# Performance work log

Measured on AMD Instinct MI355X. Metric: run time of the kernel, lower is better.

Reference implementation:

```python
import jax, jax.numpy as jnp
import numpy as np


def setup_inputs() -> dict:
    key = jax.random.key(0)
    ks = jax.random.split(key, 6)
    B, S, D_IN, D_OUT = 4, 2048, 1024, 1024
    return {
        "inputs_for_keys": jax.random.normal(ks[0], (B, S, D_IN), dtype=jnp.float32),
        "inputs_for_values": jax.random.normal(ks[1], (B, S, D_IN), dtype=jnp.float32),
        "inputs_for_queries": jax.random.normal(ks[2], (B, S, D_IN), dtype=jnp.float32),
        "K_weight": jax.random.normal(ks[3], (D_IN, D_OUT), dtype=jnp.float32) * 0.1,
        "V_weight": jax.random.normal(ks[4], (D_IN, D_OUT), dtype=jnp.float32) * 0.1,
        "Q_weight": jax.random.normal(ks[5], (D_IN, D_OUT), dtype=jnp.float32) * 0.1,
    }


def reference(inputs_for_keys, inputs_for_values, inputs_for_queries,
              K_weight, V_weight, Q_weight):
    # QKV projections: [B,S,D_in] @ [D_in,D_out] -> [B,S,D_out]
    K = jnp.einsum("bsi,io->bso", inputs_for_keys, K_weight)
    V = jnp.einsum("bsi,io->bso", inputs_for_values, V_weight)
    Q = jnp.einsum("bsi,io->bso", inputs_for_queries, Q_weight)

    Sq, Sk, d = Q.shape[1], K.shape[1], K.shape[2]
    scale = 1.0 / jnp.sqrt(jnp.asarray(d, dtype=Q.dtype))
    # scaled dot-product scores: [B, Sq, Sk]
    scores = jnp.einsum("bqd,bkd->bqk", Q, K) * scale
    # causal mask: -inf strictly above the diagonal (key index > query index)
    causal = jnp.where(jnp.arange(Sk)[None, :] > jnp.arange(Sq)[:, None],
                       jnp.float32(-jnp.inf), jnp.float32(0.0))
    scores = scores + causal[None, :, :]
    probs = jax.nn.softmax(scores, axis=-1)
    return jnp.einsum("bqk,bkd->bqd", probs, V)
```

## Files before the change

kernel.cpp:

```cpp
#include <hip/hip_runtime.h>
#include <math.h>

using f32x4  = __attribute__((ext_vector_type(4))) float;
using bf16x8 = __attribute__((ext_vector_type(8))) short;
using f16x8  = __attribute__((ext_vector_type(8))) _Float16;
using u16x8  = __attribute__((ext_vector_type(8))) unsigned short;
using u16x4  = __attribute__((ext_vector_type(4))) unsigned short;

static __device__ __forceinline__ unsigned short f2bf(float f) {
  unsigned int u = __builtin_bit_cast(unsigned int, f);
  u += 0x7FFFu + ((u >> 16) & 1u);
  return (unsigned short)(u >> 16);
}
static __device__ __forceinline__ float bf2f(unsigned short h) {
  unsigned int u = ((unsigned int)h) << 16;
  return __builtin_bit_cast(float, u);
}
static __device__ __forceinline__ unsigned short f2h(float f) {
  _Float16 h = (_Float16)f;
  return __builtin_bit_cast(unsigned short, h);
}

template <bool F16>
static __device__ __forceinline__ f32x4 mfma16(bf16x8 a, bf16x8 b, f32x4 c) {
  if constexpr (F16)
    return __builtin_amdgcn_mfma_f32_16x16x32_f16(
        __builtin_bit_cast(f16x8, a), __builtin_bit_cast(f16x8, b), c, 0, 0, 0);
  else
    return __builtin_amdgcn_mfma_f32_16x16x32_bf16(a, b, c, 0, 0, 0);
}
template <bool F16>
static __device__ __forceinline__ unsigned short cvt16(float v) {
  if constexpr (F16) return f2h(v);
  else return f2bf(v);
}

static __device__ __forceinline__ void gll16(const void* g, void* l) {
  using GPtr = const unsigned int __attribute__((address_space(1)))*;
  using LPtr = unsigned int __attribute__((address_space(3)))*;
  __builtin_amdgcn_global_load_lds((GPtr)(unsigned long long)g,
                                   (LPtr)(unsigned)(unsigned long long)l,
                                   16, 0, 0);
}

template <int BK>
static __device__ __forceinline__ void stageT(unsigned short* sdst,
                                              const unsigned short* g,
                                              size_t ld, int k0, int wave,
                                              int lane) {
  if constexpr (BK == 64) {
    const int r = lane >> 3, c8 = lane & 7;
    const int scol = (c8 ^ r) << 3;
#pragma unroll
    for (int i = 0; i < 4; ++i)
      gll16(g + (size_t)(wave * 32 + i * 8 + r) * ld + (k0 + scol),
            sdst + wave * 2048 + i * 512);
  } else {
    const int p = lane & 7;
    const int ll = lane >> 3;
#pragma unroll
    for (int i = 0; i < 2; ++i) {
      const int line = wave * 16 + i * 8 + ll;
      const int q = p ^ (line & 7);
      const int srow = 2 * line + (q >> 2);
      const int scol = (q & 3) << 3;
      gll16(g + (size_t)srow * ld + (k0 + scol), sdst + wave * 1024 + i * 512);
    }
  }
}

template <int BK>
static __device__ __forceinline__ bf16x8 fragT(const unsigned short* s,
                                               int row, int kko) {
  if constexpr (BK == 64) {
    return *(const bf16x8*)&s[row * 64 + (kko ^ ((row & 7) << 3))];
  } else {
    const int line = row >> 1;
    const int q = ((row & 1) << 2) | (kko >> 3);
    const int p = q ^ (line & 7);
    return *(const bf16x8*)&s[line * 64 + p * 8];
  }
}

__global__ __launch_bounds__(256) void convert_wkq_kernel(
    const float* __restrict__ Wk, const float* __restrict__ Wq,
    unsigned short* __restrict__ Wkh, unsigned short* __restrict__ Wqh) {
  const int z = blockIdx.z;
  const float* W = z ? Wq : Wk;
  unsigned short* H = z ? Wqh : Wkh;
  const size_t base = (size_t)blockIdx.x * 4096 + threadIdx.x * 4;
#pragma unroll
  for (int k = 0; k < 4; ++k) {
    f32x4 v = *(const f32x4*)&W[base + k * 1024];
    u16x4 h;
#pragma unroll
    for (int e = 0; e < 4; ++e) h[e] = f2h(v[e]);
    *(u16x4*)&H[base + k * 1024] = h;
  }
}

__global__ __launch_bounds__(256) void convert_wv_kernel(
    const float* __restrict__ Wv, unsigned short* __restrict__ WvT) {
  __shared__ float sW[64][65];
  const int ti = blockIdx.x * 64;
  const int tj = blockIdx.y * 64;
  const int tid = threadIdx.x;
#pragma unroll
  for (int it = 0; it < 4; ++it) {
    int idx = tid + it * 256;
    int r = idx >> 4, c = (idx & 15) << 2;
    f32x4 v = *(const f32x4*)&Wv[(size_t)(ti + r) * 1024 + tj + c];
    sW[r][c] = v[0]; sW[r][c + 1] = v[1]; sW[r][c + 2] = v[2]; sW[r][c + 3] = v[3];
  }
  __syncthreads();
#pragma unroll
  for (int it = 0; it < 4; ++it) {
    int idx = tid + it * 256;
    int ro = idx >> 4, ci = (idx & 15) << 2;
    u16x4 h;
#pragma unroll
    for (int e = 0; e < 4; ++e) h[e] = f2h(sW[ci + e][ro]);
    *(u16x4*)&WvT[(size_t)(tj + ro) * 1024 + ti + ci] = h;
  }
}

__global__ __launch_bounds__(256) void convert_x_kernel(
    const float* __restrict__ Xk, const float* __restrict__ Xq,
    const float* __restrict__ Xv, unsigned short* __restrict__ Xkh,
    unsigned short* __restrict__ Xqh, unsigned short* __restrict__ Xvh) {
  const int z = blockIdx.z;
  const float* X = (z == 0) ? Xk : (z == 1) ? Xq : Xv;
  unsigned short* H = (z == 0) ? Xkh : (z == 1) ? Xqh : Xvh;
  const size_t base = (size_t)blockIdx.x * 4096 + threadIdx.x * 4;
#pragma unroll
  for (int k = 0; k < 4; ++k) {
    f32x4 v = *(const f32x4*)&X[base + k * 1024];
    u16x4 h;
#pragma unroll
    for (int e = 0; e < 4; ++e) h[e] = f2h(v[e]);
    *(u16x4*)&H[base + k * 1024] = h;
  }
}

template <int NTERMS, int EPI, bool PACKED, bool PVK, bool F16>
__global__ __launch_bounds__(256, 2) void gemm_db_kernel(
    const unsigned short* __restrict__ Ah, const unsigned short* __restrict__ Al,
    const unsigned short* __restrict__ Bh, const unsigned short* __restrict__ Bl,
    size_t lda, size_t ldb, int K,
    float* __restrict__ Cf, unsigned short* __restrict__ Ch,
    unsigned short* __restrict__ Cl, size_t ldc,
    size_t abatch, size_t bbatch, size_t cbatch) {
  constexpr int BK = (NTERMS >= 2) ? 32 : 64;
  constexpr int NTILES = (NTERMS == 3) ? 4 : (NTERMS == 2) ? 3 : 2;
  constexpr int TILE = 128 * BK;
  __shared__ unsigned short smem[2][NTILES * TILE];

  int lid = blockIdx.x + gridDim.x * (blockIdx.y + gridDim.y * blockIdx.z);
  {
    const int n = gridDim.x * gridDim.y * gridDim.z;
    const int q = n >> 3, r = n & 7, x = lid & 7, k = lid >> 3;
    lid = (x < r ? x * (q + 1) : r * (q + 1) + (x - r) * q) + k;
  }
  int bm, bn, b;
  if constexpr (PACKED) {
    const int t = lid % gridDim.x;
    b = lid / gridDim.x;
    bm = (int)((sqrtf(8.f * (float)t + 1.f) - 1.f) * 0.5f);
    while ((bm + 1) * (bm + 2) / 2 <= t) ++bm;
    while (bm * (bm + 1) / 2 > t) --bm;
    bn = t - bm * (bm + 1) / 2;
  } else {
    bn = lid % gridDim.x;
    const int tmp = lid / gridDim.x;
    bm = tmp % gridDim.y;
    b = tmp / gridDim.y;
    if constexpr (PVK) bm = (int)gridDim.y - 1 - bm;
  }
  const int tid = threadIdx.x, lane = tid & 63, wave = tid >> 6;
  const unsigned short* gA = Ah + abatch * b + (size_t)(bm * 128) * lda;
  const unsigned short* gB = Bh + bbatch * b + (size_t)(bn * 128) * ldb;
  const unsigned short* gAl2 =
      (NTERMS == 3) ? Al + abatch * b + (size_t)(bm * 128) * lda : nullptr;
  const unsigned short* gBl2 =
      (NTERMS >= 2) ? Bl + bbatch * b + (size_t)(bn * 128) * ldb : nullptr;
  const int kend = PVK ? (bm + 1) * 128 : K;
  const int nsteps = kend / BK;
  f32x4 acc[4][4] = {};
  const int wr = (wave >> 1) << 6, wc = (wave & 1) << 6;
  const int frow = lane & 15, koff = (lane >> 4) << 3;

  auto stage_all = [&](unsigned short* buf, int k0) {
    stageT<BK>(buf, gA, lda, k0, wave, lane);
    stageT<BK>(buf + TILE, gB, ldb, k0, wave, lane);
    if constexpr (NTERMS >= 2) stageT<BK>(buf + 2 * TILE, gBl2, ldb, k0, wave, lane);
    if constexpr (NTERMS == 3) stageT<BK>(buf + 3 * TILE, gAl2, lda, k0, wave, lane);
  };

  stage_all(smem[0], 0);
  if (nsteps > 1) stage_all(smem[1], BK);
  int cur = 0;
  for (int st = 0; st < nsteps; ++st) {
    if (st + 1 < nsteps) {
      if constexpr (NTERMS == 2)
        asm volatile("s_waitcnt vmcnt(6)" ::: "memory");
      else
        asm volatile("s_waitcnt vmcnt(8)" ::: "memory");
    } else {
      asm volatile("s_waitcnt vmcnt(0)" ::: "memory");
    }
    __builtin_amdgcn_sched_barrier(0);
    __builtin_amdgcn_s_barrier();
    __builtin_amdgcn_sched_barrier(0);
    const unsigned short* sA = smem[cur];
    const unsigned short* sB = smem[cur] + TILE;
    if constexpr (NTERMS >= 2) {
      const unsigned short* sBl = smem[cur] + 2 * TILE;
      const unsigned short* sAl = smem[cur] + 3 * TILE;
      bf16x8 fBh[4], fBl[4];
#pragma unroll
      for (int j = 0; j < 4; ++j) {
        fBh[j] = fragT<BK>(sB, wc + j * 16 + frow, koff);
        fBl[j] = fragT<BK>(sBl, wc + j * 16 + frow, koff);
      }
#pragma unroll
      for (int i = 0; i < 4; ++i) {
        const bf16x8 ah = fragT<BK>(sA, wr + i * 16 + frow, koff);
        bf16x8 al = {};
        if constexpr (NTERMS == 3) al = fragT<BK>(sAl, wr + i * 16 + frow, koff);
#pragma unroll
        for (int j = 0; j < 4; ++j) {
          acc[i][j] = mfma16<F16>(ah, fBh[j], acc[i][j]);
          acc[i][j] = mfma16<F16>(ah, fBl[j], acc[i][j]);
          if constexpr (NTERMS == 3)
            acc[i][j] = mfma16<F16>(al, fBh[j], acc[i][j]);
        }
      }
    } else {
#pragma unroll
      for (int kk = 0; kk < 64; kk += 32) {
        const int kko = kk + koff;
        bf16x8 fBh[4];
#pragma unroll
        for (int j = 0; j < 4; ++j) fBh[j] = fragT<BK>(sB, wc + j * 16 + frow, kko);
#pragma unroll
        for (int i = 0; i < 4; ++i) {
          const bf16x8 ah = fragT<BK>(sA, wr + i * 16 + frow, kko);
#pragma unroll
          for (int j = 0; j < 4; ++j)
            acc[i][j] = mfma16<F16>(ah, fBh[j], acc[i][j]);
        }
      }
    }
    asm volatile("s_waitcnt lgkmcnt(0)" ::: "memory");
    __builtin_amdgcn_sched_barrier(0);
    __builtin_amdgcn_s_barrier();
    __builtin_amdgcn_sched_barrier(0);
    if (st + 2 < nsteps) stage_all(smem[cur], (st + 2) * BK);
    cur ^= 1;
  }

  const int erow = bm * 128 + wr + ((lane >> 4) << 2);
  const int ecol = bn * 128 + wc + frow;
  if constexpr (EPI == 0) {
    float* C = Cf + cbatch * b;
#pragma unroll
    for (int i = 0; i < 4; ++i)
#pragma unroll
      for (int j = 0; j < 4; ++j)
#pragma unroll
        for (int e = 0; e < 4; ++e)
          C[(size_t)(erow + i * 16 + e) * ldc + (ecol + j * 16)] = acc[i][j][e];
  } else if constexpr (EPI == 3) {
#pragma unroll
    for (int i = 0; i < 4; ++i)
#pragma unroll
      for (int j = 0; j < 4; ++j) {
        const int s = erow + i * 16;
        const int o = ecol + j * 16;
        u16x4 v;
#pragma unroll
        for (int e = 0; e < 4; ++e) v[e] = cvt16<F16>(acc[i][j][e]);
        *(u16x4*)&Ch[((size_t)(s >> 11) * 1024 + o) * 2048 + (s & 2047)] = v;
      }
  } else {
    unsigned short* Cho = Ch + cbatch * b;
    unsigned short* Clo = (EPI == 1) ? Cl + cbatch * b : nullptr;
#pragma unroll
    for (int i = 0; i < 4; ++i)
#pragma unroll
      for (int j = 0; j < 4; ++j)
#pragma unroll
        for (int e = 0; e < 4; ++e) {
          size_t off = (size_t)(erow + i * 16 + e) * ldc + (ecol + j * 16);
          float v = acc[i][j][e];
          unsigned short hh = cvt16<F16>(v);
          Cho[off] = hh;
          if constexpr (EPI == 1) Clo[off] = f2bf(v - bf2f(hh));
        }
  }
}

__global__ __launch_bounds__(256) void reduce_mt_kernel(
    const float* __restrict__ P, unsigned short* __restrict__ H) {
  const size_t base = ((size_t)blockIdx.x * 256 + threadIdx.x) * 4;
  f32x4 s = *(const f32x4*)&P[base];
#pragma unroll
  for (int z = 1; z < 4; ++z) {
    f32x4 v = *(const f32x4*)&P[(size_t)z * 1048576 + base];
    s[0] += v[0]; s[1] += v[1]; s[2] += v[2]; s[3] += v[3];
  }
  u16x4 h;
#pragma unroll
  for (int e = 0; e < 4; ++e) h[e] = f2h(s[e]);
  *(u16x4*)&H[base] = h;
}

__global__ __launch_bounds__(256) void softmax_kernel(float* __restrict__ Sc) {
  const int row = blockIdx.x;
  const int q = row & 2047;
  const int tid = threadIdx.x, lane = tid & 63, wave = tid >> 6;
  float* srow = Sc + (size_t)row * 2048;
  unsigned short* prow = (unsigned short*)srow;
  const int k0 = tid * 4, k1 = 1024 + tid * 4;
  f32x4 v0 = {}, v1 = {};
  if (k0 <= q) v0 = *(const f32x4*)(srow + k0);
  if (k1 <= q) v1 = *(const f32x4*)(srow + k1);
  float m = -3.0e38f;
#pragma unroll
  for (int e = 0; e < 4; ++e) {
    if (k0 + e <= q) m = fmaxf(m, v0[e]);
    if (k1 + e <= q) m = fmaxf(m, v1[e]);
  }
#pragma unroll
  for (int o = 32; o; o >>= 1) m = fmaxf(m, __shfl_xor(m, o));
  __shared__ float redm[4], reds[4];
  if (lane == 0) redm[wave] = m;
  __syncthreads();
  m = fmaxf(fmaxf(redm[0], redm[1]), fmaxf(redm[2], redm[3]));
  const float scale = 0.03125f;
  float p[8];
  float s = 0.f;
#pragma unroll
  for (int e = 0; e < 4; ++e) {
    p[e] = (k0 + e <= q) ? __expf((v0[e] - m) * scale) : 0.f;
    p[4 + e] = (k1 + e <= q) ? __expf((v1[e] - m) * scale) : 0.f;
    s += p[e] + p[4 + e];
  }
#pragma unroll
  for (int o = 32; o; o >>= 1) s += __shfl_xor(s, o);
  if (lane == 0) reds[wave] = s;
  __syncthreads();
  s = reds[0] + reds[1] + reds[2] + reds[3];
  const float inv = 1.0f / s;
  u16x4 o0, o1;
#pragma unroll
  for (int e = 0; e < 4; ++e) {
    o0[e] = f2h(p[e] * inv);
    o1[e] = f2h(p[4 + e] * inv);
  }
  *(u16x4*)&prow[k0] = o0;
  *(u16x4*)&prow[k1] = o1;
}

extern "C" void kernel_launch(void* const* d_in, const int* in_sizes, int n_in,
                              void* d_out, int out_size, void* d_ws, size_t ws_size,
                              hipStream_t stream) {
  const float* Xk = (const float*)d_in[0];
  const float* Xv = (const float*)d_in[1];
  const float* Xq = (const float*)d_in[2];
  const float* Wk = (const float*)d_in[3];
  const float* Wv = (const float*)d_in[4];
  const float* Wq = (const float*)d_in[5];
  float* out = (float*)d_out;

  char* ws = (char*)d_ws;
  const size_t MB = 1024ull * 1024;
  unsigned short* Xqh   = (unsigned short*)(ws + 0);
  unsigned short* Xvh   = (unsigned short*)(ws + 16 * MB);
  unsigned short* Wkh   = (unsigned short*)(ws + 32 * MB);
  unsigned short* Wqh   = (unsigned short*)(ws + 34 * MB);
  unsigned short* MTh   = (unsigned short*)(ws + 40 * MB);
  unsigned short* WvT   = (unsigned short*)(ws + 44 * MB);
  float*          MTpart= (float*)(ws + 46 * MB);
  unsigned short* Xkh   = (unsigned short*)(ws + 64 * MB);
  unsigned short* Th    = (unsigned short*)(ws + 80 * MB);
  unsigned short* VT    = (unsigned short*)(ws + 96 * MB);
  float*          Sc    = (float*)(ws + 0);

  convert_wkq_kernel<<<dim3(256, 1, 2), 256, 0, stream>>>(Wk, Wq, Wkh, Wqh);
  convert_wv_kernel<<<dim3(16, 16), 256, 0, stream>>>(Wv, WvT);
  convert_x_kernel<<<dim3(2048, 1, 3), 256, 0, stream>>>(Xk, Xq, Xv, Xkh, Xqh, Xvh);

  gemm_db_kernel<1, 0, false, false, true><<<dim3(8, 8, 4), 256, 0, stream>>>(
      Wkh, nullptr, Wqh, nullptr, 1024, 1024, 256, MTpart, nullptr, nullptr,
      1024, 256, 256, (size_t)1024 * 1024);
  reduce_mt_kernel<<<dim3(1024), 256, 0, stream>>>(MTpart, MTh);

  gemm_db_kernel<1, 2, false, false, true><<<dim3(8, 64, 1), 256, 0, stream>>>(
      Xqh, nullptr, MTh, nullptr, 1024, 1024, 1024, nullptr, Th, nullptr,
      1024, 0, 0, 0);

  gemm_db_kernel<1, 3, false, false, true><<<dim3(8, 64, 1), 256, 0, stream>>>(
      Xvh, nullptr, WvT, nullptr, 1024, 1024, 1024, nullptr, VT, nullptr,
      2048, 0, 0, 0);

  gemm_db_kernel<1, 0, true, false, true><<<dim3(136, 1, 4), 256, 0, stream>>>(
      Th, nullptr, Xkh, nullptr, 1024, 1024, 1024, Sc, nullptr, nullptr, 2048,
      (size_t)2048 * 1024, (size_t)2048 * 1024, (size_t)2048 * 2048);

  softmax_kernel<<<dim3(8192), 256, 0, stream>>>(Sc);

  gemm_db_kernel<1, 0, false, true, true><<<dim3(8, 16, 4), 256, 0, stream>>>(
      (const unsigned short*)Sc, nullptr, VT, nullptr, 4096, 2048, 2048,
      out, nullptr, nullptr, 1024, (size_t)2048 * 4096, (size_t)1024 * 2048,
      (size_t)2048 * 1024);
}
```

Baseline: 164.4 us.

## Give each wave private LDS slices to drop block-wide barriers in GEMM

Result: slower. 250.7 us (+52.5%).

```diff
diff --git a/kernel.cpp b/kernel.cpp
--- a/kernel.cpp
+++ b/kernel.cpp
@@ -2,37 +2,17 @@
 #include <math.h>
 
 using f32x4  = __attribute__((ext_vector_type(4))) float;
-using bf16x8 = __attribute__((ext_vector_type(8))) short;
 using f16x8  = __attribute__((ext_vector_type(8))) _Float16;
 using u16x8  = __attribute__((ext_vector_type(8))) unsigned short;
 using u16x4  = __attribute__((ext_vector_type(4))) unsigned short;
 
-static __device__ __forceinline__ unsigned short f2bf(float f) {
-  unsigned int u = __builtin_bit_cast(unsigned int, f);
-  u += 0x7FFFu + ((u >> 16) & 1u);
-  return (unsigned short)(u >> 16);
-}
-static __device__ __forceinline__ float bf2f(unsigned short h) {
-  unsigned int u = ((unsigned int)h) << 16;
-  return __builtin_bit_cast(float, u);
-}
 static __device__ __forceinline__ unsigned short f2h(float f) {
   _Float16 h = (_Float16)f;
   return __builtin_bit_cast(unsigned short, h);
 }
 
-template <bool F16>
-static __device__ __forceinline__ f32x4 mfma16(bf16x8 a, bf16x8 b, f32x4 c) {
-  if constexpr (F16)
-    return __builtin_amdgcn_mfma_f32_16x16x32_f16(
-        __builtin_bit_cast(f16x8, a), __builtin_bit_cast(f16x8, b), c, 0, 0, 0);
-  else
-    return __builtin_amdgcn_mfma_f32_16x16x32_bf16(a, b, c, 0, 0, 0);
-}
-template <bool F16>
-static __device__ __forceinline__ unsigned short cvt16(float v) {
-  if constexpr (F16) return f2h(v);
-  else return f2bf(v);
+static __device__ __forceinline__ f32x4 mfma_f16(f16x8 a, f16x8 b, f32x4 c) {
+  return __builtin_amdgcn_mfma_f32_16x16x32_f16(a, b, c, 0, 0, 0);
 }
 
 static __device__ __forceinline__ void gll16(const void* g, void* l) {
@@ -43,43 +23,25 @@
                                    16, 0, 0);
 }
 
-template <int BK>
-static __device__ __forceinline__ void stageT(unsigned short* sdst,
-                                              const unsigned short* g,
-                                              size_t ld, int k0, int wave,
-                                              int lane) {
-  if constexpr (BK == 64) {
-    const int r = lane >> 3, c8 = lane & 7;
-    const int scol = (c8 ^ r) << 3;
-#pragma unroll
-    for (int i = 0; i < 4; ++i)
-      gll16(g + (size_t)(wave * 32 + i * 8 + r) * ld + (k0 + scol),
-            sdst + wave * 2048 + i * 512);
-  } else {
-    const int p = lane & 7;
-    const int ll = lane >> 3;
-#pragma unroll
-    for (int i = 0; i < 2; ++i) {
-      const int line = wave * 16 + i * 8 + ll;
-      const int q = p ^ (line & 7);
-      const int srow = 2 * line + (q >> 2);
-      const int scol = (q & 3) << 3;
-      gll16(g + (size_t)srow * ld + (k0 + scol), sdst + wave * 1024 + i * 512);
-    }
-  }
-}
-
-template <int BK>
-static __device__ __forceinline__ bf16x8 fragT(const unsigned short* s,
-                                               int row, int kko) {
-  if constexpr (BK == 64) {
-    return *(const bf16x8*)&s[row * 64 + (kko ^ ((row & 7) << 3))];
-  } else {
-    const int line = row >> 1;
-    const int q = ((row & 1) << 2) | (kko >> 3);
-    const int p = q ^ (line & 7);
-    return *(const bf16x8*)&s[line * 64 + p * 8];
-  }
+static __device__ __forceinline__ void stage_slice(unsigned short* dst,
+                                                   const unsigned short* g,
+                                                   size_t ld, int k0, int lane) {
+  const int p = lane & 7, ll = lane >> 3;
+#pragma unroll
+  for (int i = 0; i < 4; ++i) {
+    const int line = i * 8 + ll;
+    const int q = p ^ (line & 7);
+    gll16(g + (size_t)(2 * line + (q >> 2)) * ld + (k0 + ((q & 3) << 3)),
+          dst + i * 512);
+  }
+}
+
+static __device__ __forceinline__ f16x8 frag_slice(const unsigned short* s,
+                                                   int row, int kko) {
+  const int line = row >> 1;
+  const int q = ((row & 1) << 2) | (kko >> 3);
+  const int p = q ^ (line & 7);
+  return *(const f16x8*)&s[line * 64 + p * 8];
 }
 
 __global__ __launch_bounds__(256) void convert_wkq_kernel(
@@ -142,18 +104,13 @@
   }
 }
 
-template <int NTERMS, int EPI, bool PACKED, bool PVK, bool F16>
-__global__ __launch_bounds__(256, 2) void gemm_db_kernel(
-    const unsigned short* __restrict__ Ah, const unsigned short* __restrict__ Al,
-    const unsigned short* __restrict__ Bh, const unsigned short* __restrict__ Bl,
+template <int EPI, bool PACKED, bool PVK>
+__global__ __launch_bounds__(256, 2) void gemm_pw_kernel(
+    const unsigned short* __restrict__ Ah, const unsigned short* __restrict__ Bh,
     size_t lda, size_t ldb, int K,
-    float* __restrict__ Cf, unsigned short* __restrict__ Ch,
-    unsigned short* __restrict__ Cl, size_t ldc,
+    float* __restrict__ Cf, unsigned short* __restrict__ Ch, size_t ldc,
     size_t abatch, size_t bbatch, size_t cbatch) {
-  constexpr int BK = (NTERMS >= 2) ? 32 : 64;
-  constexpr int NTILES = (NTERMS == 3) ? 4 : (NTERMS == 2) ? 3 : 2;
-  constexpr int TILE = 128 * BK;
-  __shared__ unsigned short smem[2][NTILES * TILE];
+  __shared__ unsigned short smem[2][4][4096];
 
   int lid = blockIdx.x + gridDim.x * (blockIdx.y + gridDim.y * blockIdx.z);
   {
@@ -177,85 +134,43 @@
     if constexpr (PVK) bm = (int)gridDim.y - 1 - bm;
   }
   const int tid = threadIdx.x, lane = tid & 63, wave = tid >> 6;
-  const unsigned short* gA = Ah + abatch * b + (size_t)(bm * 128) * lda;
-  const unsigned short* gB = Bh + bbatch * b + (size_t)(bn * 128) * ldb;
-  const unsigned short* gAl2 =
-      (NTERMS == 3) ? Al + abatch * b + (size_t)(bm * 128) * lda : nullptr;
-  const unsigned short* gBl2 =
-      (NTERMS >= 2) ? Bl + bbatch * b + (size_t)(bn * 128) * ldb : nullptr;
+  const int wr = (wave >> 1) << 6, wc = (wave & 1) << 6;
+  const unsigned short* gA = Ah + abatch * b + (size_t)(bm * 128 + wr) * lda;
+  const unsigned short* gB = Bh + bbatch * b + (size_t)(bn * 128 + wc) * ldb;
   const int kend = PVK ? (bm + 1) * 128 : K;
-  const int nsteps = kend / BK;
+  const int nsteps = kend / 32;
   f32x4 acc[4][4] = {};
-  const int wr = (wave >> 1) << 6, wc = (wave & 1) << 6;
   const int frow = lane & 15, koff = (lane >> 4) << 3;
 
-  auto stage_all = [&](unsigned short* buf, int k0) {
-    stageT<BK>(buf, gA, lda, k0, wave, lane);
-    stageT<BK>(buf + TILE, gB, ldb, k0, wave, lane);
-    if constexpr (NTERMS >= 2) stageT<BK>(buf + 2 * TILE, gBl2, ldb, k0, wave, lane);
-    if constexpr (NTERMS == 3) stageT<BK>(buf + 3 * TILE, gAl2, lda, k0, wave, lane);
+  unsigned short* myA[2] = {&smem[0][wave][0], &smem[1][wave][0]};
+  unsigned short* myB[2] = {&smem[0][wave][2048], &smem[1][wave][2048]};
+  auto stage_all = [&](int buf, int k0) {
+    stage_slice(myA[buf], gA, lda, k0, lane);
+    stage_slice(myB[buf], gB, ldb, k0, lane);
   };
 
-  stage_all(smem[0], 0);
-  if (nsteps > 1) stage_all(smem[1], BK);
+  stage_all(0, 0);
+  stage_all(1, 32);
   int cur = 0;
   for (int st = 0; st < nsteps; ++st) {
     if (st + 1 < nsteps) {
-      if constexpr (NTERMS == 2)
-        asm volatile("s_waitcnt vmcnt(6)" ::: "memory");
-      else
-        asm volatile("s_waitcnt vmcnt(8)" ::: "memory");
+      asm volatile("s_waitcnt vmcnt(8)" ::: "memory");
     } else {
       asm volatile("s_waitcnt vmcnt(0)" ::: "memory");
     }
     __builtin_amdgcn_sched_barrier(0);
-    __builtin_amdgcn_s_barrier();
-    __builtin_amdgcn_sched_barrier(0);
-    const unsigned short* sA = smem[cur];
-    const unsigned short* sB = smem[cur] + TILE;
-    if constexpr (NTERMS >= 2) {
-      const unsigned short* sBl = smem[cur] + 2 * TILE;
-      const unsigned short* sAl = smem[cur] + 3 * TILE;
-      bf16x8 fBh[4], fBl[4];
-#pragma unroll
-      for (int j = 0; j < 4; ++j) {
-        fBh[j] = fragT<BK>(sB, wc + j * 16 + frow, koff);
-        fBl[j] = fragT<BK>(sBl, wc + j * 16 + frow, koff);
-      }
-#pragma unroll
-      for (int i = 0; i < 4; ++i) {
-        const bf16x8 ah = fragT<BK>(sA, wr + i * 16 + frow, koff);
-        bf16x8 al = {};
-        if constexpr (NTERMS == 3) al = fragT<BK>(sAl, wr + i * 16 + frow, koff);
-#pragma unroll
-        for (int j = 0; j < 4; ++j) {
-          acc[i][j] = mfma16<F16>(ah, fBh[j], acc[i][j]);
-          acc[i][j] = mfma16<F16>(ah, fBl[j], acc[i][j]);
-          if constexpr (NTERMS == 3)
-            acc[i][j] = mfma16<F16>(al, fBh[j], acc[i][j]);
-        }
-      }
-    } else {
-#pragma unroll
-      for (int kk = 0; kk < 64; kk += 32) {
-        const int kko = kk + koff;
-        bf16x8 fBh[4];
-#pragma unroll
-        for (int j = 0; j < 4; ++j) fBh[j] = fragT<BK>(sB, wc + j * 16 + frow, kko);
-#pragma unroll
-        for (int i = 0; i < 4; ++i) {
-          const bf16x8 ah = fragT<BK>(sA, wr + i * 16 + frow, kko);
-#pragma unroll
-          for (int j = 0; j < 4; ++j)
-            acc[i][j] = mfma16<F16>(ah, fBh[j], acc[i][j]);
-        }
-      }
+    f16x8 fB[4];
+#pragma unroll
+    for (int j = 0; j < 4; ++j) fB[j] = frag_slice(myB[cur], j * 16 + frow, koff);
+#pragma unroll
+    for (int i = 0; i < 4; ++i) {
+      const f16x8 a = frag_slice(myA[cur], i * 16 + frow, koff);
+#pragma unroll
+      for (int j = 0; j < 4; ++j) acc[i][j] = mfma_f16(a, fB[j], acc[i][j]);
     }
     asm volatile("s_waitcnt lgkmcnt(0)" ::: "memory");
     __builtin_amdgcn_sched_barrier(0);
-    __builtin_amdgcn_s_barrier();
-    __builtin_amdgcn_sched_barrier(0);
-    if (st + 2 < nsteps) stage_all(smem[cur], (st + 2) * BK);
+    if (st + 2 < nsteps) stage_all(cur, (st + 2) * 32);
     cur ^= 1;
   }
 
@@ -279,24 +194,19 @@
         const int o = ecol + j * 16;
         u16x4 v;
 #pragma unroll
-        for (int e = 0; e < 4; ++e) v[e] = cvt16<F16>(acc[i][j][e]);
+        for (int e = 0; e < 4; ++e) v[e] = f2h(acc[i][j][e]);
         *(u16x4*)&Ch[((size_t)(s >> 11) * 1024 + o) * 2048 + (s & 2047)] = v;
       }
   } else {
     unsigned short* Cho = Ch + cbatch * b;
-    unsigned short* Clo = (EPI == 1) ? Cl + cbatch * b : nullptr;
 #pragma unroll
     for (int i = 0; i < 4; ++i)
 #pragma unroll
       for (int j = 0; j < 4; ++j)
 #pragma unroll
-        for (int e = 0; e < 4; ++e) {
-          size_t off = (size_t)(erow + i * 16 + e) * ldc + (ecol + j * 16);
-          float v = acc[i][j][e];
-          unsigned short hh = cvt16<F16>(v);
-          Cho[off] = hh;
-          if constexpr (EPI == 1) Clo[off] = f2bf(v - bf2f(hh));
-        }
+        for (int e = 0; e < 4; ++e)
+          Cho[(size_t)(erow + i * 16 + e) * ldc + (ecol + j * 16)] =
+              f2h(acc[i][j][e]);
   }
 }
 
@@ -391,27 +301,24 @@
   convert_wv_kernel<<<dim3(16, 16), 256, 0, stream>>>(Wv, WvT);
   convert_x_kernel<<<dim3(2048, 1, 3), 256, 0, stream>>>(Xk, Xq, Xv, Xkh, Xqh, Xvh);
 
-  gemm_db_kernel<1, 0, false, false, true><<<dim3(8, 8, 4), 256, 0, stream>>>(
-      Wkh, nullptr, Wqh, nullptr, 1024, 1024, 256, MTpart, nullptr, nullptr,
-      1024, 256, 256, (size_t)1024 * 1024);
+  gemm_pw_kernel<0, false, false><<<dim3(8, 8, 4), 256, 0, stream>>>(
+      Wkh, Wqh, 1024, 1024, 256, MTpart, nullptr, 1024, 256, 256,
+      (size_t)1024 * 1024);
   reduce_mt_kernel<<<dim3(1024), 256, 0, stream>>>(MTpart, MTh);
 
-  gemm_db_kernel<1, 2, false, false, true><<<dim3(8, 64, 1), 256, 0, stream>>>(
-      Xqh, nullptr, MTh, nullptr, 1024, 1024, 1024, nullptr, Th, nullptr,
-      1024, 0, 0, 0);
-
-  gemm_db_kernel<1, 3, false, false, true><<<dim3(8, 64, 1), 256, 0, stream>>>(
-      Xvh, nullptr, WvT, nullptr, 1024, 1024, 1024, nullptr, VT, nullptr,
-      2048, 0, 0, 0);
-
-  gemm_db_kernel<1, 0, true, false, true><<<dim3(136, 1, 4), 256, 0, stream>>>(
-      Th, nullptr, Xkh, nullptr, 1024, 1024, 1024, Sc, nullptr, nullptr, 2048,
-      (size_t)2048 * 1024, (size_t)2048 * 1024, (size_t)2048 * 2048);
+  gemm_pw_kernel<2, false, false><<<dim3(8, 64, 1), 256, 0, stream>>>(
+      Xqh, MTh, 1024, 1024, 1024, nullptr, Th, 1024, 0, 0, 0);
+
+  gemm_pw_kernel<3, false, false><<<dim3(8, 64, 1), 256, 0, stream>>>(
+      Xvh, WvT, 1024, 1024, 1024, nullptr, VT, 2048, 0, 0, 0);
+
+  gemm_pw_kernel<0, true, false><<<dim3(136, 1, 4), 256, 0, stream>>>(
+      Th, Xkh, 1024, 1024, 1024, Sc, nullptr, 2048, (size_t)2048 * 1024,
+      (size_t)2048 * 1024, (size_t)2048 * 2048);
 
   softmax_kernel<<<dim3(8192), 256, 0, stream>>>(Sc);
 
-  gemm_db_kernel<1, 0, false, true, true><<<dim3(8, 16, 4), 256, 0, stream>>>(
-      (const unsigned short*)Sc, nullptr, VT, nullptr, 4096, 2048, 2048,
-      out, nullptr, nullptr, 1024, (size_t)2048 * 4096, (size_t)1024 * 2048,
-      (size_t)2048 * 1024);
-}
+  gemm_pw_kernel<0, false, true><<<dim3(8, 16, 4), 256, 0, stream>>>(
+      (const unsigned short*)Sc, VT, 4096, 2048, 2048, out, nullptr, 1024,
+      (size_t)2048 * 4096, (size_t)1024 * 2048, (size_t)2048 * 1024);
+}
```
